# Kernel tuning notes

Hardware: AMD Instinct MI355X
Metric: run time of the kernel (lower is better)

The kernel has to match this reference:

```python
import jax, jax.numpy as jnp
import numpy as np

DIM = 1024
N_HEADS = 16
HEAD_DIM = DIM // N_HEADS
FREQS = [31.0, 37.0, 41.0, 43.0, 47.0]
TWO_PI = 2.0 * float(np.pi)


def setup_inputs() -> dict:
    key = jax.random.key(0)
    ks = jax.random.split(key, 16)
    B, L = 2, 1024
    s = 0.02
    inp = {
        'x': jax.random.normal(ks[0], (B, L, DIM), dtype=jnp.float32),
        'Wq': jax.random.normal(ks[1], (DIM, DIM), dtype=jnp.float32) * s,
        'bq': jnp.zeros((DIM,), dtype=jnp.float32),
        'Wk': jax.random.normal(ks[2], (DIM, DIM), dtype=jnp.float32) * s,
        'bk': jnp.zeros((DIM,), dtype=jnp.float32),
        'Wv': jax.random.normal(ks[3], (DIM, DIM), dtype=jnp.float32) * s,
        'bv': jnp.zeros((DIM,), dtype=jnp.float32),
        'Wo': jax.random.normal(ks[4], (DIM, DIM), dtype=jnp.float32) * s,
        'bo': jnp.zeros((DIM,), dtype=jnp.float32),
        'alpha': jax.random.normal(ks[5], (N_HEADS, len(FREQS)), dtype=jnp.float32) * 0.1,
        'phi': jax.random.uniform(ks[6], (N_HEADS, len(FREQS)), dtype=jnp.float32) * TWO_PI,
        'temperature': jnp.ones((1,), dtype=jnp.float32),
        'gamma': jnp.ones((DIM,), dtype=jnp.float32),
        'beta': jnp.zeros((DIM,), dtype=jnp.float32),
    }
    return inp


def reference(x, Wq, bq, Wk, bk, Wv, bv, Wo, bo, alpha, phi, temperature, gamma, beta):
    B, L, D = x.shape
    H, hd = N_HEADS, HEAD_DIM
    # projections (torch Linear: y = x @ W.T + b), split heads -> (B,H,L,hd)
    q = (x @ Wq.T + bq).reshape(B, L, H, hd).transpose(0, 2, 1, 3)
    k = (x @ Wk.T + bk).reshape(B, L, H, hd).transpose(0, 2, 1, 3)
    v = (x @ Wv.T + bv).reshape(B, L, H, hd).transpose(0, 2, 1, 3)
    # similarity (B,H,L,L)
    sim = jnp.einsum('bhid,bhjd->bhij', q, k) / jnp.sqrt(jnp.asarray(hd, x.dtype))
    temp = jnp.abs(temperature)[0] + 0.1
    sim = sim / temp
    # multi-frequency holographic scores: sum_f alpha_f * sin(2*pi*sim/p_f + phi_f)
    scores = jnp.zeros_like(sim)
    for fi, freq in enumerate(FREQS):
        a = alpha[:, fi][None, :, None, None]
        p = phi[:, fi][None, :, None, None]
        scores = scores + a * jnp.sin(TWO_PI * sim / freq + p)
    # sigmoid-sum normalization (not softmax)
    w = jax.nn.sigmoid(scores)
    w = w / (jnp.sum(w, axis=-1, keepdims=True) + 1e-10)
    out = jnp.einsum('bhij,bhjd->bhid', w, v)
    out = out.transpose(0, 2, 1, 3).reshape(B, L, D)
    out = out @ Wo.T + bo
    # LayerNorm (eps=1e-5, biased variance)
    mu = jnp.mean(out, axis=-1, keepdims=True)
    var = jnp.mean(jnp.square(out - mu), axis=-1, keepdims=True)
    return (out - mu) / jnp.sqrt(var + 1e-5) * gamma + beta
```

## Files before the change

### kernel.cpp

```cpp
#include <hip/hip_runtime.h>
#include <hip/hip_bf16.h>

typedef short bf16x8 __attribute__((ext_vector_type(8)));
typedef float f32x4 __attribute__((ext_vector_type(4)));

#define MFMA16(a, b, c) __builtin_amdgcn_mfma_f32_16x16x32_bf16(a, b, c, 0, 0, 0)

static constexpr int SEQ = 1024;
static constexpr int DIM = 1024;
static constexpr int NH = 16;
static constexpr int HD = 64;

#if __has_builtin(__builtin_amdgcn_sinf)
#define SIN_REV(x) __builtin_amdgcn_sinf(x)
#else
#define SIN_REV(x) __sinf((x) * 6.28318530718f)
#endif

#if __has_builtin(__builtin_amdgcn_rcpf)
#define FAST_RCP(x) __builtin_amdgcn_rcpf(x)
#else
#define FAST_RCP(x) (1.0f / (x))
#endif

__device__ __forceinline__ void stage16(const __hip_bfloat16* g, __hip_bfloat16* l, int lane) {
#if __has_builtin(__builtin_amdgcn_global_load_lds)
    __builtin_amdgcn_global_load_lds(
        (const __attribute__((address_space(1))) unsigned int*)g,
        (__attribute__((address_space(3))) unsigned int*)l, 16, 0, 0);
#else
    *(bf16x8*)(l + lane * 8) = *(const bf16x8*)g;
#endif
}

__device__ __forceinline__ int swz(int r) { return r ^ (r >> 3); }

__global__ __launch_bounds__(256) void cvt_all(
    const float* __restrict__ x,  const float* __restrict__ wq,
    const float* __restrict__ wk, const float* __restrict__ wv,
    const float* __restrict__ wo,
    __hip_bfloat16* __restrict__ xb,  __hip_bfloat16* __restrict__ wqb,
    __hip_bfloat16* __restrict__ wkb, __hip_bfloat16* __restrict__ wvb,
    __hip_bfloat16* __restrict__ wob)
{
    const int reg = blockIdx.y;
    const float* src; __hip_bfloat16* dst; int n;
    if      (reg == 0) { src = x;  dst = xb;  n = 2 * SEQ * DIM; }
    else if (reg == 1) { src = wq; dst = wqb; n = DIM * DIM; }
    else if (reg == 2) { src = wk; dst = wkb; n = DIM * DIM; }
    else if (reg == 3) { src = wv; dst = wvb; n = DIM * DIM; }
    else               { src = wo; dst = wob; n = DIM * DIM; }
    const int i = (blockIdx.x * 256 + threadIdx.x) * 4;
    if (i < n) {
        float4 v = *(const float4*)(src + i);
        __hip_bfloat16 t[4];
        t[0] = __float2bfloat16(v.x); t[1] = __float2bfloat16(v.y);
        t[2] = __float2bfloat16(v.z); t[3] = __float2bfloat16(v.w);
        *(ushort4*)(dst + i) = *(ushort4*)t;
    }
}

template <typename OutT>
__global__ __launch_bounds__(256) void gemm128(
    const __hip_bfloat16* __restrict__ A,
    const __hip_bfloat16* __restrict__ W0, const __hip_bfloat16* __restrict__ W1,
    const __hip_bfloat16* __restrict__ W2,
    const float* __restrict__ b0, const float* __restrict__ b1,
    const float* __restrict__ b2,
    OutT* __restrict__ Y0, OutT* __restrict__ Y1, OutT* __restrict__ Y2,
    int M, int N, int K)
{
    __shared__ __align__(16) __hip_bfloat16 As[128 * 32];
    __shared__ __align__(16) __hip_bfloat16 Bs[128 * 32];

    const int z = blockIdx.z;
    const __hip_bfloat16* W = (z == 0) ? W0 : ((z == 1) ? W1 : W2);
    const float* bias = (z == 0) ? b0 : ((z == 1) ? b1 : b2);
    OutT* Y = (z == 0) ? Y0 : ((z == 1) ? Y1 : Y2);

    const int tid = threadIdx.x;
    const int wv = tid >> 6, lane = tid & 63;
    const int col16 = lane & 15, quad = lane >> 4;
    const int m0 = blockIdx.x * 128, n0 = blockIdx.y * 128;

    const int c0i = (wv * 2) * 64 + lane, c1i = (wv * 2 + 1) * 64 + lane;
    const __hip_bfloat16* ga0 = A + (size_t)(m0 + (c0i >> 2)) * K + (c0i & 3) * 8;
    const __hip_bfloat16* ga1 = A + (size_t)(m0 + (c1i >> 2)) * K + (c1i & 3) * 8;
    const __hip_bfloat16* gb0 = W + (size_t)(n0 + (c0i >> 2)) * K + (c0i & 3) * 8;
    const __hip_bfloat16* gb1 = W + (size_t)(n0 + (c1i >> 2)) * K + (c1i & 3) * 8;
    __hip_bfloat16* la0 = As + (wv * 2) * 512;
    __hip_bfloat16* la1 = As + (wv * 2 + 1) * 512;
    __hip_bfloat16* lb0 = Bs + (wv * 2) * 512;
    __hip_bfloat16* lb1 = Bs + (wv * 2 + 1) * 512;

    const int wr = wv >> 1, wc = wv & 1;
    const __hip_bfloat16* ar = As + (wr * 64 + col16) * 32 + quad * 8;
    const __hip_bfloat16* br = Bs + (wc * 64 + col16) * 32 + quad * 8;

    f32x4 acc[16] = {};

    for (int k0 = 0; k0 < K; k0 += 32) {
        __syncthreads();
        stage16(ga0 + k0, la0, lane);
        stage16(ga1 + k0, la1, lane);
        stage16(gb0 + k0, lb0, lane);
        stage16(gb1 + k0, lb1, lane);
        __syncthreads();
        bf16x8 af[4], bfm[4];
#pragma unroll
        for (int mt = 0; mt < 4; ++mt) af[mt] = *(const bf16x8*)(ar + mt * 16 * 32);
#pragma unroll
        for (int nt = 0; nt < 4; ++nt) bfm[nt] = *(const bf16x8*)(br + nt * 16 * 32);
#pragma unroll
        for (int mt = 0; mt < 4; ++mt)
#pragma unroll
            for (int nt = 0; nt < 4; ++nt)
                acc[mt * 4 + nt] = MFMA16(af[mt], bfm[nt], acc[mt * 4 + nt]);
    }

#pragma unroll
    for (int nt = 0; nt < 4; ++nt) {
        const int n = n0 + wc * 64 + nt * 16 + col16;
        const float bv = bias[n];
#pragma unroll
        for (int mt = 0; mt < 4; ++mt) {
#pragma unroll
            for (int r = 0; r < 4; ++r) {
                const int m = m0 + wr * 64 + mt * 16 + quad * 4 + r;
                Y[(size_t)m * N + n] = (OutT)(acc[mt * 4 + nt][r] + bv);
            }
        }
    }
}

__global__ __launch_bounds__(256) void attn_kernel(
    const __hip_bfloat16* __restrict__ Q,
    const __hip_bfloat16* __restrict__ K,
    const __hip_bfloat16* __restrict__ V,
    const float* __restrict__ alpha, const float* __restrict__ phi,
    const float* __restrict__ temperature,
    __hip_bfloat16* __restrict__ AO)
{
    __shared__ __align__(16) char smem[18432 + 5120];
    __hip_bfloat16* VtBase = (__hip_bfloat16*)smem;
    __hip_bfloat16* PlBase = (__hip_bfloat16*)(smem + 18432);
    float* Ocomb = (float*)smem;
    float* Dl    = (float*)(smem + 2 * 16 * 68 * 4);

    const int tid = threadIdx.x;
    const int wv = tid >> 6, lane = tid & 63;
    const int col16 = lane & 15, quad = lane >> 4;
    const int g = wv & 1, half = wv >> 1;

    const int bh = blockIdx.y, b = bh >> 4, h = bh & 15;
    const int i0 = blockIdx.x * 32 + g * 16;
    const size_t base = ((size_t)b * SEQ) * DIM + (size_t)h * HD;

    const float tempv = fabsf(temperature[0]) + 0.1f;
    const float simscale = 1.0f / (8.0f * tempv);
    const float freqs[5] = {31.0f, 37.0f, 41.0f, 43.0f, 47.0f};
    float al[5], prev[5], crev[5];
#pragma unroll
    for (int f = 0; f < 5; ++f) {
        al[f]   = alpha[h * 5 + f];
        prev[f] = phi[h * 5 + f] * 0.15915494309f;
        crev[f] = simscale / freqs[f];
    }

    const __hip_bfloat16* qrow = Q + base + (size_t)(i0 + col16) * DIM + quad * 8;
    const bf16x8 qa0 = *(const bf16x8*)(qrow);
    const bf16x8 qa1 = *(const bf16x8*)(qrow + 32);

    const int tl = tid & 127;
    const int sc0 = (tl & 7) * 8;
    const int sx  = tl & 7;
    const int jj0 = (tl >> 3) * 2;
    __hip_bfloat16* VtH = VtBase + half * 64 * 72;
    __hip_bfloat16* rowp[8];
#pragma unroll
    for (int e = 0; e < 8; ++e) rowp[e] = VtH + (sc0 + (e ^ sx)) * 72;

    const __hip_bfloat16* vrd[4];
#pragma unroll
    for (int t = 0; t < 4; ++t)
        vrd[t] = VtH + swz(t * 16 + col16) * 72 + quad * 8;

    __hip_bfloat16* PlW = PlBase + wv * 16 * 40;
    const __hip_bfloat16* plr = PlW + swz(col16) * 40 + quad * 8;
    __hip_bfloat16* plw[4];
#pragma unroll
    for (int r = 0; r < 4; ++r) plw[r] = PlW + swz(quad * 4 + r) * 40;

    f32x4 o[4] = {};
    float denom[4] = {0.f, 0.f, 0.f, 0.f};

    for (int it = 0; it < 8; ++it) {
        const int j0 = half * 512 + it * 64;
        __syncthreads();
#pragma unroll
        for (int s = 0; s < 2; ++s) {
            const __hip_bfloat16* vp = V + base + (size_t)(j0 + jj0 + 32 * s) * DIM + sc0;
            bf16x8 va = *(const bf16x8*)(vp);
            bf16x8 vb2 = *(const bf16x8*)(vp + DIM);
#pragma unroll
            for (int e = 0; e < 8; ++e) {
                unsigned pk = ((unsigned)(unsigned short)va[e]) |
                              (((unsigned)(unsigned short)vb2[e]) << 16);
                *(unsigned*)(rowp[e] + jj0 + 32 * s) = pk;
            }
        }
        __syncthreads();

#pragma unroll
        for (int sub = 0; sub < 2; ++sub) {
#pragma unroll
            for (int s2 = 0; s2 < 2; ++s2) {
                const int js = j0 + (sub * 2 + s2) * 16;
                const __hip_bfloat16* krow = K + base + (size_t)(js + col16) * DIM + quad * 8;
                bf16x8 kb0 = *(const bf16x8*)(krow);
                bf16x8 kb1 = *(const bf16x8*)(krow + 32);
                f32x4 sa = {};
                sa = MFMA16(qa0, kb0, sa);
                sa = MFMA16(qa1, kb1, sa);
#pragma unroll
                for (int r = 0; r < 4; ++r) {
                    float sc = 0.f;
#pragma unroll
                    for (int f = 0; f < 5; ++f)
                        sc += al[f] * SIN_REV(sa[r] * crev[f] + prev[f]);
                    const float w = FAST_RCP(1.0f + __expf(-sc));
                    denom[r] += w;
                    plw[r][s2 * 16 + col16] = __float2bfloat16(w);
                }
            }
            bf16x8 pa = *(const bf16x8*)plr;
#pragma unroll
            for (int t = 0; t < 4; ++t) {
                bf16x8 vb = *(const bf16x8*)(vrd[t] + 32 * sub);
                o[t] = MFMA16(pa, vb, o[t]);
            }
        }
    }

#pragma unroll
    for (int r = 0; r < 4; ++r) {
        float d = denom[r];
        d += __shfl_xor(d, 1);
        d += __shfl_xor(d, 2);
        d += __shfl_xor(d, 4);
        d += __shfl_xor(d, 8);
        denom[r] = d;
    }

    __syncthreads();
    if (half == 1) {
#pragma unroll
        for (int t = 0; t < 4; ++t)
#pragma unroll
            for (int r = 0; r < 4; ++r)
                Ocomb[(g * 16 + quad * 4 + r) * 68 + t * 16 + col16] = o[t][r];
        if (col16 == 0) {
#pragma unroll
            for (int r = 0; r < 4; ++r) Dl[g * 16 + quad * 4 + r] = denom[r];
        }
    }
    __syncthreads();
    if (half == 0) {
#pragma unroll
        for (int r = 0; r < 4; ++r)
            denom[r] = denom[r] + Dl[g * 16 + quad * 4 + r] + 1e-10f;
#pragma unroll
        for (int t = 0; t < 4; ++t) {
#pragma unroll
            for (int r = 0; r < 4; ++r) {
                const float val =
                    (o[t][r] + Ocomb[(g * 16 + quad * 4 + r) * 68 + t * 16 + col16]) / denom[r];
                const size_t row = (size_t)b * SEQ + i0 + quad * 4 + r;
                AO[row * DIM + h * HD + t * 16 + col16] = __float2bfloat16(val);
            }
        }
    }
}

__global__ __launch_bounds__(256) void ln_kernel(
    const float* __restrict__ Yp,
    const float* __restrict__ gamma,
    const float* __restrict__ beta,
    float* __restrict__ out)
{
    const int row = blockIdx.x;
    const float* y = Yp + (size_t)row * DIM;

    float v[4];
    float s = 0.f, s2 = 0.f;
#pragma unroll
    for (int e = 0; e < 4; ++e) {
        v[e] = y[threadIdx.x + e * 256];
        s += v[e];
        s2 += v[e] * v[e];
    }
#pragma unroll
    for (int off = 1; off < 64; off <<= 1) {
        s  += __shfl_xor(s, off);
        s2 += __shfl_xor(s2, off);
    }
    __shared__ float ps[4], ps2[4];
    const int wave = threadIdx.x >> 6;
    if ((threadIdx.x & 63) == 0) { ps[wave] = s; ps2[wave] = s2; }
    __syncthreads();
    s  = ps[0] + ps[1] + ps[2] + ps[3];
    s2 = ps2[0] + ps2[1] + ps2[2] + ps2[3];

    const float mu   = s * (1.0f / DIM);
    const float var  = s2 * (1.0f / DIM) - mu * mu;
    const float rstd = rsqrtf(var + 1e-5f);

#pragma unroll
    for (int e = 0; e < 4; ++e) {
        const int idx = threadIdx.x + e * 256;
        out[(size_t)row * DIM + idx] =
            (v[e] - mu) * rstd * gamma[idx] + beta[idx];
    }
}

extern "C" void kernel_launch(void* const* d_in, const int* in_sizes, int n_in,
                              void* d_out, int out_size, void* d_ws, size_t ws_size,
                              hipStream_t stream)
{
    const float* x     = (const float*)d_in[0];
    const float* Wq    = (const float*)d_in[1];
    const float* bq    = (const float*)d_in[2];
    const float* Wk    = (const float*)d_in[3];
    const float* bk    = (const float*)d_in[4];
    const float* Wv    = (const float*)d_in[5];
    const float* bv    = (const float*)d_in[6];
    const float* Wo    = (const float*)d_in[7];
    const float* bo    = (const float*)d_in[8];
    const float* alpha = (const float*)d_in[9];
    const float* phi   = (const float*)d_in[10];
    const float* temp  = (const float*)d_in[11];
    const float* gamma = (const float*)d_in[12];
    const float* beta  = (const float*)d_in[13];

    float* out = (float*)d_out;

    const int B = 2;
    const int M = B * SEQ;

    char* wsb = (char*)d_ws;
    __hip_bfloat16* xb  = (__hip_bfloat16*)(wsb + 0);
    __hip_bfloat16* Wqb = (__hip_bfloat16*)(wsb + (4u  << 20));
    __hip_bfloat16* Wkb = (__hip_bfloat16*)(wsb + (6u  << 20));
    __hip_bfloat16* Wvb = (__hip_bfloat16*)(wsb + (8u  << 20));
    __hip_bfloat16* Wob = (__hip_bfloat16*)(wsb + (10u << 20));
    __hip_bfloat16* Qb  = (__hip_bfloat16*)(wsb + (12u << 20));
    __hip_bfloat16* Kb  = (__hip_bfloat16*)(wsb + (16u << 20));
    __hip_bfloat16* Vb  = (__hip_bfloat16*)(wsb + (20u << 20));
    __hip_bfloat16* AO  = (__hip_bfloat16*)(wsb + (24u << 20));
    float*          Yp  = (float*)(wsb + 0);

    hipLaunchKernelGGL(cvt_all, dim3(2048, 5), dim3(256), 0, stream,
                       x, Wq, Wk, Wv, Wo, xb, Wqb, Wkb, Wvb, Wob);

    hipLaunchKernelGGL((gemm128<__hip_bfloat16>), dim3(M / 128, DIM / 128, 3), dim3(256), 0, stream,
                       xb, Wqb, Wkb, Wvb, bq, bk, bv, Qb, Kb, Vb, M, DIM, DIM);

    hipLaunchKernelGGL(attn_kernel, dim3(SEQ / 32, B * NH), dim3(256), 0, stream,
                       Qb, Kb, Vb, alpha, phi, temp, AO);

    hipLaunchKernelGGL((gemm128<float>), dim3(M / 128, DIM / 128, 1), dim3(256), 0, stream,
                       AO, Wob, Wob, Wob, bo, bo, bo, Yp, Yp, Yp, M, DIM, DIM);

    hipLaunchKernelGGL(ln_kernel, dim3(M), dim3(256), 0, stream, Yp, gamma, beta, out);
}
```

Baseline: 198.2 us.

## Shrink GEMM tiles, split-K output projection, prefetch K tiles, use exp2 sigmoid

The QKV GEMM now uses 64x128 tiles, giving twice as many blocks so more of the CUs are busy. The output projection is split along K into two partial sums, and the LayerNorm kernel adds them together, which raises the block count for that GEMM too. The attention kernel loads all four K fragments for each 64-key tile before the barrier, so the loads overlap the V transpose. It also folds log2(e) into alpha so the sigmoid can use a hardware exp2. In exchange there is extra partial-sum traffic through global memory and more register use in attention.

```diff
diff --git a/kernel.cpp b/kernel.cpp
--- a/kernel.cpp
+++ b/kernel.cpp
@@ -21,6 +21,12 @@
 #define FAST_RCP(x) __builtin_amdgcn_rcpf(x)
 #else
 #define FAST_RCP(x) (1.0f / (x))
+#endif
+
+#if __has_builtin(__builtin_amdgcn_exp2f)
+#define EXP2F(x) __builtin_amdgcn_exp2f(x)
+#else
+#define EXP2F(x) exp2f(x)
 #endif
 
 __device__ __forceinline__ void stage16(const __hip_bfloat16* g, __hip_bfloat16* l, int lane) {
@@ -60,59 +66,57 @@
     }
 }
 
-template <typename OutT>
-__global__ __launch_bounds__(256) void gemm128(
+__global__ __launch_bounds__(256) void gemm_qkv(
     const __hip_bfloat16* __restrict__ A,
     const __hip_bfloat16* __restrict__ W0, const __hip_bfloat16* __restrict__ W1,
     const __hip_bfloat16* __restrict__ W2,
     const float* __restrict__ b0, const float* __restrict__ b1,
     const float* __restrict__ b2,
-    OutT* __restrict__ Y0, OutT* __restrict__ Y1, OutT* __restrict__ Y2,
+    __hip_bfloat16* __restrict__ Y0, __hip_bfloat16* __restrict__ Y1,
+    __hip_bfloat16* __restrict__ Y2,
     int M, int N, int K)
 {
-    __shared__ __align__(16) __hip_bfloat16 As[128 * 32];
-    __shared__ __align__(16) __hip_bfloat16 Bs[128 * 32];
+    __shared__ __align__(16) __hip_bfloat16 As[64 * 32];
+    __shared__ __align__(16) __hip_bfloat16 Ws[128 * 32];
 
     const int z = blockIdx.z;
     const __hip_bfloat16* W = (z == 0) ? W0 : ((z == 1) ? W1 : W2);
     const float* bias = (z == 0) ? b0 : ((z == 1) ? b1 : b2);
-    OutT* Y = (z == 0) ? Y0 : ((z == 1) ? Y1 : Y2);
+    __hip_bfloat16* Y = (z == 0) ? Y0 : ((z == 1) ? Y1 : Y2);
 
     const int tid = threadIdx.x;
     const int wv = tid >> 6, lane = tid & 63;
     const int col16 = lane & 15, quad = lane >> 4;
-    const int m0 = blockIdx.x * 128, n0 = blockIdx.y * 128;
-
-    const int c0i = (wv * 2) * 64 + lane, c1i = (wv * 2 + 1) * 64 + lane;
-    const __hip_bfloat16* ga0 = A + (size_t)(m0 + (c0i >> 2)) * K + (c0i & 3) * 8;
-    const __hip_bfloat16* ga1 = A + (size_t)(m0 + (c1i >> 2)) * K + (c1i & 3) * 8;
-    const __hip_bfloat16* gb0 = W + (size_t)(n0 + (c0i >> 2)) * K + (c0i & 3) * 8;
-    const __hip_bfloat16* gb1 = W + (size_t)(n0 + (c1i >> 2)) * K + (c1i & 3) * 8;
-    __hip_bfloat16* la0 = As + (wv * 2) * 512;
-    __hip_bfloat16* la1 = As + (wv * 2 + 1) * 512;
-    __hip_bfloat16* lb0 = Bs + (wv * 2) * 512;
-    __hip_bfloat16* lb1 = Bs + (wv * 2 + 1) * 512;
+    const int m0 = blockIdx.x * 64, n0 = blockIdx.y * 128;
+
+    const int ca = wv * 64 + lane;
+    const int cb0 = ca, cb1 = 256 + ca;
+    const __hip_bfloat16* ga  = A + (size_t)(m0 + (ca  >> 2)) * K + (ca  & 3) * 8;
+    const __hip_bfloat16* gb0 = W + (size_t)(n0 + (cb0 >> 2)) * K + (cb0 & 3) * 8;
+    const __hip_bfloat16* gb1 = W + (size_t)(n0 + (cb1 >> 2)) * K + (cb1 & 3) * 8;
+    __hip_bfloat16* la  = As + wv * 512;
+    __hip_bfloat16* lb0 = Ws + wv * 512;
+    __hip_bfloat16* lb1 = Ws + 2048 + wv * 512;
 
     const int wr = wv >> 1, wc = wv & 1;
-    const __hip_bfloat16* ar = As + (wr * 64 + col16) * 32 + quad * 8;
-    const __hip_bfloat16* br = Bs + (wc * 64 + col16) * 32 + quad * 8;
-
-    f32x4 acc[16] = {};
+    const __hip_bfloat16* ar = As + (wr * 32 + col16) * 32 + quad * 8;
+    const __hip_bfloat16* br = Ws + (wc * 64 + col16) * 32 + quad * 8;
+
+    f32x4 acc[8] = {};
 
     for (int k0 = 0; k0 < K; k0 += 32) {
         __syncthreads();
-        stage16(ga0 + k0, la0, lane);
-        stage16(ga1 + k0, la1, lane);
+        stage16(ga  + k0, la,  lane);
         stage16(gb0 + k0, lb0, lane);
         stage16(gb1 + k0, lb1, lane);
         __syncthreads();
-        bf16x8 af[4], bfm[4];
-#pragma unroll
-        for (int mt = 0; mt < 4; ++mt) af[mt] = *(const bf16x8*)(ar + mt * 16 * 32);
+        bf16x8 af[2], bfm[4];
+#pragma unroll
+        for (int mt = 0; mt < 2; ++mt) af[mt] = *(const bf16x8*)(ar + mt * 16 * 32);
 #pragma unroll
         for (int nt = 0; nt < 4; ++nt) bfm[nt] = *(const bf16x8*)(br + nt * 16 * 32);
 #pragma unroll
-        for (int mt = 0; mt < 4; ++mt)
+        for (int mt = 0; mt < 2; ++mt)
 #pragma unroll
             for (int nt = 0; nt < 4; ++nt)
                 acc[mt * 4 + nt] = MFMA16(af[mt], bfm[nt], acc[mt * 4 + nt]);
@@ -123,11 +127,78 @@
         const int n = n0 + wc * 64 + nt * 16 + col16;
         const float bv = bias[n];
 #pragma unroll
-        for (int mt = 0; mt < 4; ++mt) {
+        for (int mt = 0; mt < 2; ++mt) {
 #pragma unroll
             for (int r = 0; r < 4; ++r) {
-                const int m = m0 + wr * 64 + mt * 16 + quad * 4 + r;
-                Y[(size_t)m * N + n] = (OutT)(acc[mt * 4 + nt][r] + bv);
+                const int m = m0 + wr * 32 + mt * 16 + quad * 4 + r;
+                Y[(size_t)m * N + n] = __float2bfloat16(acc[mt * 4 + nt][r] + bv);
+            }
+        }
+    }
+}
+
+__global__ __launch_bounds__(256) void gemm_osplit(
+    const __hip_bfloat16* __restrict__ A,
+    const __hip_bfloat16* __restrict__ W,
+    const float* __restrict__ bias,
+    float* __restrict__ Y0, float* __restrict__ Y1,
+    int M, int N, int K)
+{
+    __shared__ __align__(16) __hip_bfloat16 As[64 * 32];
+    __shared__ __align__(16) __hip_bfloat16 Ws[128 * 32];
+
+    const int z = blockIdx.z;
+    float* Y = (z == 0) ? Y0 : Y1;
+    const int kb = z * 512;
+
+    const int tid = threadIdx.x;
+    const int wv = tid >> 6, lane = tid & 63;
+    const int col16 = lane & 15, quad = lane >> 4;
+    const int m0 = blockIdx.x * 64, n0 = blockIdx.y * 128;
+
+    const int ca = wv * 64 + lane;
+    const int cb1 = 256 + ca;
+    const __hip_bfloat16* ga  = A + (size_t)(m0 + (ca  >> 2)) * K + (ca  & 3) * 8 + kb;
+    const __hip_bfloat16* gb0 = W + (size_t)(n0 + (ca  >> 2)) * K + (ca  & 3) * 8 + kb;
+    const __hip_bfloat16* gb1 = W + (size_t)(n0 + (cb1 >> 2)) * K + (cb1 & 3) * 8 + kb;
+    __hip_bfloat16* la  = As + wv * 512;
+    __hip_bfloat16* lb0 = Ws + wv * 512;
+    __hip_bfloat16* lb1 = Ws + 2048 + wv * 512;
+
+    const int wr = wv >> 1, wc = wv & 1;
+    const __hip_bfloat16* ar = As + (wr * 32 + col16) * 32 + quad * 8;
+    const __hip_bfloat16* br = Ws + (wc * 64 + col16) * 32 + quad * 8;
+
+    f32x4 acc[8] = {};
+
+    for (int k0 = 0; k0 < 512; k0 += 32) {
+        __syncthreads();
+        stage16(ga  + k0, la,  lane);
+        stage16(gb0 + k0, lb0, lane);
+        stage16(gb1 + k0, lb1, lane);
+        __syncthreads();
+        bf16x8 af[2], bfm[4];
+#pragma unroll
+        for (int mt = 0; mt < 2; ++mt) af[mt] = *(const bf16x8*)(ar + mt * 16 * 32);
+#pragma unroll
+        for (int nt = 0; nt < 4; ++nt) bfm[nt] = *(const bf16x8*)(br + nt * 16 * 32);
+#pragma unroll
+        for (int mt = 0; mt < 2; ++mt)
+#pragma unroll
+            for (int nt = 0; nt < 4; ++nt)
+                acc[mt * 4 + nt] = MFMA16(af[mt], bfm[nt], acc[mt * 4 + nt]);
+    }
+
+#pragma unroll
+    for (int nt = 0; nt < 4; ++nt) {
+        const int n = n0 + wc * 64 + nt * 16 + col16;
+        const float bv = (z == 0) ? bias[n] : 0.0f;
+#pragma unroll
+        for (int mt = 0; mt < 2; ++mt) {
+#pragma unroll
+            for (int r = 0; r < 4; ++r) {
+                const int m = m0 + wr * 32 + mt * 16 + quad * 4 + r;
+                Y[(size_t)m * N + n] = acc[mt * 4 + nt][r] + bv;
             }
         }
     }
@@ -162,7 +233,7 @@
     float al[5], prev[5], crev[5];
 #pragma unroll
     for (int f = 0; f < 5; ++f) {
-        al[f]   = alpha[h * 5 + f];
+        al[f]   = alpha[h * 5 + f] * 1.44269504089f;
         prev[f] = phi[h * 5 + f] * 0.15915494309f;
         crev[f] = simscale / freqs[f];
     }
@@ -170,6 +241,8 @@
     const __hip_bfloat16* qrow = Q + base + (size_t)(i0 + col16) * DIM + quad * 8;
     const bf16x8 qa0 = *(const bf16x8*)(qrow);
     const bf16x8 qa1 = *(const bf16x8*)(qrow + 32);
+
+    const __hip_bfloat16* kbase = K + base + (size_t)col16 * DIM + quad * 8;
 
     const int tl = tid & 127;
     const int sc0 = (tl & 7) * 8;
@@ -200,7 +273,7 @@
 #pragma unroll
         for (int s = 0; s < 2; ++s) {
             const __hip_bfloat16* vp = V + base + (size_t)(j0 + jj0 + 32 * s) * DIM + sc0;
-            bf16x8 va = *(const bf16x8*)(vp);
+            bf16x8 va  = *(const bf16x8*)(vp);
             bf16x8 vb2 = *(const bf16x8*)(vp + DIM);
 #pragma unroll
             for (int e = 0; e < 8; ++e) {
@@ -209,26 +282,30 @@
                 *(unsigned*)(rowp[e] + jj0 + 32 * s) = pk;
             }
         }
+        bf16x8 kf[4][2];
+#pragma unroll
+        for (int u = 0; u < 4; ++u) {
+            const __hip_bfloat16* kp = kbase + (size_t)(j0 + u * 16) * DIM;
+            kf[u][0] = *(const bf16x8*)(kp);
+            kf[u][1] = *(const bf16x8*)(kp + 32);
+        }
         __syncthreads();
 
 #pragma unroll
         for (int sub = 0; sub < 2; ++sub) {
 #pragma unroll
             for (int s2 = 0; s2 < 2; ++s2) {
-                const int js = j0 + (sub * 2 + s2) * 16;
-                const __hip_bfloat16* krow = K + base + (size_t)(js + col16) * DIM + quad * 8;
-                bf16x8 kb0 = *(const bf16x8*)(krow);
-                bf16x8 kb1 = *(const bf16x8*)(krow + 32);
+                const int u = sub * 2 + s2;
                 f32x4 sa = {};
-                sa = MFMA16(qa0, kb0, sa);
-                sa = MFMA16(qa1, kb1, sa);
+                sa = MFMA16(qa0, kf[u][0], sa);
+                sa = MFMA16(qa1, kf[u][1], sa);
 #pragma unroll
                 for (int r = 0; r < 4; ++r) {
                     float sc = 0.f;
 #pragma unroll
                     for (int f = 0; f < 5; ++f)
                         sc += al[f] * SIN_REV(sa[r] * crev[f] + prev[f]);
-                    const float w = FAST_RCP(1.0f + __expf(-sc));
+                    const float w = FAST_RCP(1.0f + EXP2F(-sc));
                     denom[r] += w;
                     plw[r][s2 * 16 + col16] = __float2bfloat16(w);
                 }
@@ -283,19 +360,22 @@
 }
 
 __global__ __launch_bounds__(256) void ln_kernel(
-    const float* __restrict__ Yp,
+    const float* __restrict__ Yp0,
+    const float* __restrict__ Yp1,
     const float* __restrict__ gamma,
     const float* __restrict__ beta,
     float* __restrict__ out)
 {
     const int row = blockIdx.x;
-    const float* y = Yp + (size_t)row * DIM;
+    const float* y0 = Yp0 + (size_t)row * DIM;
+    const float* y1 = Yp1 + (size_t)row * DIM;
 
     float v[4];
     float s = 0.f, s2 = 0.f;
 #pragma unroll
     for (int e = 0; e < 4; ++e) {
-        v[e] = y[threadIdx.x + e * 256];
+        const int idx = threadIdx.x + e * 256;
+        v[e] = y0[idx] + y1[idx];
         s += v[e];
         s2 += v[e] * v[e];
     }
@@ -357,19 +437,21 @@
     __hip_bfloat16* Kb  = (__hip_bfloat16*)(wsb + (16u << 20));
     __hip_bfloat16* Vb  = (__hip_bfloat16*)(wsb + (20u << 20));
     __hip_bfloat16* AO  = (__hip_bfloat16*)(wsb + (24u << 20));
-    float*          Yp  = (float*)(wsb + 0);
+    float*          Yp0 = (float*)(wsb + 0);
+    float*          Yp1 = (float*)(wsb + (12u << 20));
 
     hipLaunchKernelGGL(cvt_all, dim3(2048, 5), dim3(256), 0, stream,
                        x, Wq, Wk, Wv, Wo, xb, Wqb, Wkb, Wvb, Wob);
 
-    hipLaunchKernelGGL((gemm128<__hip_bfloat16>), dim3(M / 128, DIM / 128, 3), dim3(256), 0, stream,
+    hipLaunchKernelGGL(gemm_qkv, dim3(M / 64, DIM / 128, 3), dim3(256), 0, stream,
                        xb, Wqb, Wkb, Wvb, bq, bk, bv, Qb, Kb, Vb, M, DIM, DIM);
 
     hipLaunchKernelGGL(attn_kernel, dim3(SEQ / 32, B * NH), dim3(256), 0, stream,
                        Qb, Kb, Vb, alpha, phi, temp, AO);
 
-    hipLaunchKernelGGL((gemm128<float>), dim3(M / 128, DIM / 128, 1), dim3(256), 0, stream,
-                       AO, Wob, Wob, Wob, bo, bo, bo, Yp, Yp, Yp, M, DIM, DIM);
-
-    hipLaunchKernelGGL(ln_kernel, dim3(M), dim3(256), 0, stream, Yp, gamma, beta, out);
-}
+    hipLaunchKernelGGL(gemm_osplit, dim3(M / 64, DIM / 128, 2), dim3(256), 0, stream,
+                       AO, Wob, bo, Yp0, Yp1, M, DIM, DIM);
+
+    hipLaunchKernelGGL(ln_kernel, dim3(M), dim3(256), 0, stream,
+                       Yp0, Yp1, gamma, beta, out);
+}
```

After: 181.3 us. 1.09x faster.
